# Kernel tuning notes

Hardware: AMD Instinct MI355X
Metric: run time of the kernel (lower is better)

The kernel has to match this reference:

```python
import jax, jax.numpy as jnp
import numpy as np

N_NODES = 50000
N_EDGES = 800000
F_IN = 256
HID = 64
HEADS = 4
NEG_SLOPE = 0.2


def setup_inputs() -> dict:
    key = jax.random.key(0)
    ks = jax.random.split(key, 12)
    x = jax.random.normal(ks[0], (N_NODES, F_IN), dtype=jnp.float32)
    src = jax.random.randint(ks[1], (N_EDGES,), 0, N_NODES)
    dst = jax.random.randint(ks[2], (N_EDGES,), 0, N_NODES)
    s0 = 1.0 / np.sqrt(F_IN)
    s1 = 1.0 / np.sqrt(HEADS * HID)
    W0 = jax.random.normal(ks[3], (F_IN, HEADS * HID), dtype=jnp.float32) * s0
    a_l0 = jax.random.normal(ks[4], (HEADS, HID), dtype=jnp.float32) * s1
    a_r0 = jax.random.normal(ks[5], (HEADS, HID), dtype=jnp.float32) * s1
    b0 = jnp.zeros((HEADS * HID,), dtype=jnp.float32)
    W1 = jax.random.normal(ks[6], (HEADS * HID, HEADS * HID), dtype=jnp.float32) * s1
    a_l1 = jax.random.normal(ks[7], (HEADS, HID), dtype=jnp.float32) * s1
    a_r1 = jax.random.normal(ks[8], (HEADS, HID), dtype=jnp.float32) * s1
    b1 = jnp.zeros((HEADS * HID,), dtype=jnp.float32)
    return {"x": x, "src": src, "dst": dst,
            "W0": W0, "a_l0": a_l0, "a_r0": a_r0, "b0": b0,
            "W1": W1, "a_l1": a_l1, "a_r1": a_r1, "b1": b1}


def _gat_layer(h, src, dst, W, a_l, a_r, b):
    # h: [N, F_in] -> feat: [N, H, D]
    feat = (h @ W).reshape(h.shape[0], HEADS, HID)
    el = jnp.sum(feat * a_l, axis=-1)  # [N, H]
    er = jnp.sum(feat * a_r, axis=-1)  # [N, H]
    e = jax.nn.leaky_relu(el[src] + er[dst], NEG_SLOPE)  # [E, H]
    # per-destination edge softmax (numerically stable)
    m = jax.ops.segment_max(e, dst, num_segments=N_NODES)  # [N, H]
    ex = jnp.exp(e - m[dst])
    s = jax.ops.segment_sum(ex, dst, num_segments=N_NODES)  # [N, H]
    alpha = ex / jnp.maximum(s[dst], 1e-9)  # [E, H]
    msg = feat[src] * alpha[:, :, None]  # [E, H, D]
    rst = jax.ops.segment_sum(msg, dst, num_segments=N_NODES)  # [N, H, D]
    rst = rst + b.reshape(1, HEADS, HID)
    return jax.nn.elu(rst)


def reference(x, src, dst, W0, a_l0, a_r0, b0, W1, a_l1, a_r1, b1):
    h = _gat_layer(x, src, dst, W0, a_l0, a_r0, b0)  # [N, H, D]
    h = h.reshape(N_NODES, HEADS * HID)              # flatten(1)
    h = _gat_layer(h, src, dst, W1, a_l1, a_r1, b1)  # [N, H, D]
    # list of per-head outputs h[:, i]
    return tuple(h[:, i] for i in range(HEADS))
```

## Files before the change

kernel.cpp:

```cpp
#include <hip/hip_runtime.h>
#include <math.h>

#define N_NODES 50000
#define N_EDGES 800000
#define HEADS 4
#define HID 64
#define FDIM 256
#define LDA 40
#define SCAN_CHUNK 1024
#define SCAN_NB ((N_NODES + SCAN_CHUNK - 1) / SCAN_CHUNK)

typedef __attribute__((ext_vector_type(8))) _Float16 half8;
typedef __attribute__((ext_vector_type(4))) _Float16 half4;
typedef __attribute__((ext_vector_type(4))) float f32x4;


__global__ __launch_bounds__(256) void hist_kernel(const int* __restrict__ dst,
                                                   int* __restrict__ counts, int E) {
    int i = blockIdx.x * blockDim.x + threadIdx.x;
    if (i < E) atomicAdd(&counts[dst[i]], 1);
}

__global__ __launch_bounds__(256) void scan_local(const int* __restrict__ counts,
                                                  int* __restrict__ offs,
                                                  int* __restrict__ bsum, int n) {
    __shared__ int part[256];
    const int b = blockIdx.x, t = threadIdx.x;
    const int base = b * SCAN_CHUNK + t * 4;
    int v[4];
#pragma unroll
    for (int j = 0; j < 4; j++) {
        int idx = base + j;
        v[j] = (idx < n) ? counts[idx] : 0;
    }
    int s0 = v[0], s1 = s0 + v[1], s2 = s1 + v[2], s3 = s2 + v[3];
    part[t] = s3;
    __syncthreads();
    for (int off = 1; off < 256; off <<= 1) {
        int x = (t >= off) ? part[t - off] : 0;
        __syncthreads();
        part[t] += x;
        __syncthreads();
    }
    int prefix = (t > 0) ? part[t - 1] : 0;
    int e[4] = {prefix, prefix + s0, prefix + s1, prefix + s2};
#pragma unroll
    for (int j = 0; j < 4; j++) {
        int idx = base + j;
        if (idx < n) offs[idx] = e[j];
    }
    if (t == 255) bsum[b] = part[255];
}

__global__ __launch_bounds__(64) void scan_bsum(int* __restrict__ bsum,
                                                int* __restrict__ offs, int nb, int n) {
    int lane = threadIdx.x;
    int own = (lane < nb) ? bsum[lane] : 0;
    int v = own;
    for (int off = 1; off < 64; off <<= 1) {
        int x = __shfl_up(v, off);
        if (lane >= off) v += x;
    }
    if (lane < nb) bsum[lane] = v - own;
    if (lane == nb - 1) offs[n] = v;
}

__global__ __launch_bounds__(256) void scan_add(int* __restrict__ offs,
                                                const int* __restrict__ bsum, int n) {
    const int b = blockIdx.x;
    const int p = bsum[b];
    const int base = b * SCAN_CHUNK + threadIdx.x * 4;
#pragma unroll
    for (int j = 0; j < 4; j++) {
        int idx = base + j;
        if (idx < n) offs[idx] += p;
    }
}

__global__ __launch_bounds__(256) void scatter_kernel(const int* __restrict__ src,
                                                      const int* __restrict__ dst,
                                                      const int* __restrict__ offs,
                                                      int* __restrict__ cursor,
                                                      int* __restrict__ csr_src, int E) {
    int i = blockIdx.x * blockDim.x + threadIdx.x;
    if (i < E) {
        int d = dst[i];
        int p = offs[d] + atomicAdd(&cursor[d], 1);
        csr_src[p] = src[i];
    }
}


__global__ __launch_bounds__(256) void wcast_kernel(const float* __restrict__ W0,
                                                    const float* __restrict__ W1,
                                                    _Float16* __restrict__ wt0,
                                                    _Float16* __restrict__ wt1) {
    const float* W = blockIdx.y ? W1 : W0;
    _Float16* wt = blockIdx.y ? wt1 : wt0;
    int n = blockIdx.x * 16 + (threadIdx.x >> 4);
    int k0 = (threadIdx.x & 15) * 16;
    for (int j = 0; j < 16; j++)
        wt[n * FDIM + k0 + j] = (_Float16)W[(k0 + j) * FDIM + n];
}

__global__ __launch_bounds__(256) void cast_x_kernel(const float* __restrict__ x,
                                                     _Float16* __restrict__ x16) {
    size_t i = ((size_t)blockIdx.x * 256 + threadIdx.x) * 4;
    float4 v = *(const float4*)&x[i];
    half4 h = {(_Float16)v.x, (_Float16)v.y, (_Float16)v.z, (_Float16)v.w};
    *(half4*)&x16[i] = h;
}

__global__ __launch_bounds__(256) void mfma_gemm(const _Float16* __restrict__ A16,
                                                 const _Float16* __restrict__ Bt,
                                                 const float* __restrict__ al,
                                                 const float* __restrict__ ar,
                                                 _Float16* __restrict__ feat16,
                                                 float* __restrict__ el,
                                                 float* __restrict__ er) {
    __shared__ _Float16 ash[128][LDA];
    __shared__ _Float16 bsh[128][LDA];

    const int t = threadIdx.x;
    const int m0 = blockIdx.x * 128;
    const int n0 = blockIdx.y * 128;
    const int wave = t >> 6, lane = t & 63;
    const int quad = lane >> 4, l16 = lane & 15;
    const int wr = (wave >> 1) * 64;
    const int wc = (wave & 1) * 64;

    const f32x4 zero = {0.f, 0.f, 0.f, 0.f};
    f32x4 acc[4][4];
#pragma unroll
    for (int i = 0; i < 4; i++)
#pragma unroll
        for (int j = 0; j < 4; j++) acc[i][j] = zero;

    for (int kk = 0; kk < FDIM; kk += 32) {
#pragma unroll
        for (int ii = 0; ii < 2; ii++) {
            int idx = t + ii * 256;
            int row = idx >> 2;
            int kb = (idx & 3) * 8;
            int gr = m0 + row; if (gr >= N_NODES) gr = N_NODES - 1;
            *(half8*)&ash[row][kb] = *(const half8*)&A16[(size_t)gr * FDIM + kk + kb];
            *(half8*)&bsh[row][kb] = *(const half8*)&Bt[(size_t)(n0 + row) * FDIM + kk + kb];
        }
        __syncthreads();

        half8 af[4], bf[4];
#pragma unroll
        for (int i = 0; i < 4; i++) {
            af[i] = *(half8*)&ash[wr + i * 16 + l16][quad * 8];
            bf[i] = *(half8*)&bsh[wc + i * 16 + l16][quad * 8];
        }
#pragma unroll
        for (int mt = 0; mt < 4; mt++)
#pragma unroll
            for (int nt = 0; nt < 4; nt++)
                acc[mt][nt] = __builtin_amdgcn_mfma_f32_16x16x32_f16(af[mt], bf[nt], acc[mt][nt], 0, 0, 0);
        __syncthreads();
    }

    const int h = (n0 + wc) >> 6;
    float alv[4], arv[4];
#pragma unroll
    for (int nt = 0; nt < 4; nt++) {
        alv[nt] = al[n0 + wc + nt * 16 + l16];
        arv[nt] = ar[n0 + wc + nt * 16 + l16];
    }
#pragma unroll
    for (int mt = 0; mt < 4; mt++) {
        int m = m0 + wr + mt * 16 + quad * 4;
        float pl[4] = {0.f, 0.f, 0.f, 0.f}, pr[4] = {0.f, 0.f, 0.f, 0.f};
#pragma unroll
        for (int nt = 0; nt < 4; nt++) {
            int n = n0 + wc + nt * 16 + l16;
#pragma unroll
            for (int r = 0; r < 4; r++) {
                float v = acc[mt][nt][r];
                if (m + r < N_NODES) feat16[(size_t)(m + r) * FDIM + n] = (_Float16)v;
                pl[r] += v * alv[nt];
                pr[r] += v * arv[nt];
            }
        }
#pragma unroll
        for (int r = 0; r < 4; r++) {
            float a = pl[r], b = pr[r];
            for (int off = 8; off; off >>= 1) {
                a += __shfl_down(a, off, 16);
                b += __shfl_down(b, off, 16);
            }
            if (l16 == 0 && m + r < N_NODES) {
                el[(m + r) * 4 + h] = a;
                er[(m + r) * 4 + h] = b;
            }
        }
    }
}

__global__ __launch_bounds__(256) void agg_fused(const _Float16* __restrict__ feat16,
                                                 const float* __restrict__ el,
                                                 const float* __restrict__ er,
                                                 const float* __restrict__ bias,
                                                 const int* __restrict__ offs,
                                                 const int* __restrict__ csr_src,
                                                 float* __restrict__ out,
                                                 _Float16* __restrict__ h1,
                                                 int mode) {
    const int wave = threadIdx.x >> 6;
    const int lane = threadIdx.x & 63;
    const int n = blockIdx.x * 4 + wave;
    const int head = lane >> 4;
    const int f = lane * 4;
    const int beg = offs[n];
    const int end = offs[n + 1];
    const float er_h = er[n * 4 + head];

    float4 acc0 = make_float4(0.f, 0.f, 0.f, 0.f);
    float4 acc1 = make_float4(0.f, 0.f, 0.f, 0.f);
    float ss0 = 0.f, ss1 = 0.f;

    int i = beg;
    for (; i + 3 < end; i += 4) {
        int s0 = csr_src[i], s1 = csr_src[i + 1];
        int s2 = csr_src[i + 2], s3 = csr_src[i + 3];
        float e0 = el[s0 * 4 + head] + er_h;
        float e1 = el[s1 * 4 + head] + er_h;
        float e2 = el[s2 * 4 + head] + er_h;
        float e3 = el[s3 * 4 + head] + er_h;
        half4 v0 = *(const half4*)&feat16[(size_t)s0 * FDIM + f];
        half4 v1 = *(const half4*)&feat16[(size_t)s1 * FDIM + f];
        half4 v2 = *(const half4*)&feat16[(size_t)s2 * FDIM + f];
        half4 v3 = *(const half4*)&feat16[(size_t)s3 * FDIM + f];
        e0 = (e0 > 0.f) ? e0 : 0.2f * e0;
        e1 = (e1 > 0.f) ? e1 : 0.2f * e1;
        e2 = (e2 > 0.f) ? e2 : 0.2f * e2;
        e3 = (e3 > 0.f) ? e3 : 0.2f * e3;
        float w0 = __expf(e0), w1 = __expf(e1), w2 = __expf(e2), w3 = __expf(e3);
        ss0 += w0 + w2;
        ss1 += w1 + w3;
        acc0.x += w0 * (float)v0[0] + w2 * (float)v2[0];
        acc0.y += w0 * (float)v0[1] + w2 * (float)v2[1];
        acc0.z += w0 * (float)v0[2] + w2 * (float)v2[2];
        acc0.w += w0 * (float)v0[3] + w2 * (float)v2[3];
        acc1.x += w1 * (float)v1[0] + w3 * (float)v3[0];
        acc1.y += w1 * (float)v1[1] + w3 * (float)v3[1];
        acc1.z += w1 * (float)v1[2] + w3 * (float)v3[2];
        acc1.w += w1 * (float)v1[3] + w3 * (float)v3[3];
    }
    for (; i < end; i++) {
        int s0 = csr_src[i];
        float e0 = el[s0 * 4 + head] + er_h;
        half4 v0 = *(const half4*)&feat16[(size_t)s0 * FDIM + f];
        e0 = (e0 > 0.f) ? e0 : 0.2f * e0;
        float w0 = __expf(e0);
        ss0 += w0;
        acc0.x += w0 * (float)v0[0];
        acc0.y += w0 * (float)v0[1];
        acc0.z += w0 * (float)v0[2];
        acc0.w += w0 * (float)v0[3];
    }

    float S = fmaxf(ss0 + ss1, 1e-9f);
    float inv = 1.f / S;
    float4 bv = *(const float4*)&bias[f];
    float r0 = (acc0.x + acc1.x) * inv + bv.x;
    float r1 = (acc0.y + acc1.y) * inv + bv.y;
    float r2 = (acc0.z + acc1.z) * inv + bv.z;
    float r3 = (acc0.w + acc1.w) * inv + bv.w;
    r0 = (r0 > 0.f) ? r0 : expm1f(r0);
    r1 = (r1 > 0.f) ? r1 : expm1f(r1);
    r2 = (r2 > 0.f) ? r2 : expm1f(r2);
    r3 = (r3 > 0.f) ? r3 : expm1f(r3);

    if (mode) {
        const int d = (lane & 15) * 4;
        float4 rv = make_float4(r0, r1, r2, r3);
        *(float4*)&out[(size_t)head * N_NODES * HID + (size_t)n * HID + d] = rv;
    } else {
        half4 hv = {(_Float16)r0, (_Float16)r1, (_Float16)r2, (_Float16)r3};
        *(half4*)&h1[(size_t)n * FDIM + f] = hv;
    }
}


extern "C" void kernel_launch(void* const* d_in, const int* in_sizes, int n_in,
                              void* d_out, int out_size, void* d_ws, size_t ws_size,
                              hipStream_t stream) {
    const float* x   = (const float*)d_in[0];
    const int*   src = (const int*)d_in[1];
    const int*   dst = (const int*)d_in[2];
    const float* W0  = (const float*)d_in[3];
    const float* al0 = (const float*)d_in[4];
    const float* ar0 = (const float*)d_in[5];
    const float* b0  = (const float*)d_in[6];
    const float* W1  = (const float*)d_in[7];
    const float* al1 = (const float*)d_in[8];
    const float* ar1 = (const float*)d_in[9];
    const float* b1  = (const float*)d_in[10];
    float* out = (float*)d_out;

    _Float16* x16h1 = (_Float16*)d_out;

    _Float16* feat16 = (_Float16*)d_ws;
    _Float16* wt0 = feat16 + (size_t)N_NODES * FDIM;
    _Float16* wt1 = wt0 + FDIM * FDIM;
    float* el    = (float*)(wt1 + FDIM * FDIM);
    float* er    = el + N_NODES * HEADS;
    int* counts  = (int*)(er + N_NODES * HEADS);
    int* cursor  = counts + N_NODES;
    int* offs    = cursor + N_NODES;
    int* bsum    = offs + 50016;
    int* csr_src = bsum + 64;

    hipMemsetAsync(counts, 0, 2 * N_NODES * sizeof(int), stream);
    wcast_kernel<<<dim3(16, 2), 256, 0, stream>>>(W0, W1, wt0, wt1);
    cast_x_kernel<<<N_NODES * FDIM / 1024, 256, 0, stream>>>(x, x16h1);
    hist_kernel<<<(N_EDGES + 255) / 256, 256, 0, stream>>>(dst, counts, N_EDGES);
    scan_local<<<SCAN_NB, 256, 0, stream>>>(counts, offs, bsum, N_NODES);
    scan_bsum<<<1, 64, 0, stream>>>(bsum, offs, SCAN_NB, N_NODES);
    scan_add<<<SCAN_NB, 256, 0, stream>>>(offs, bsum, N_NODES);
    scatter_kernel<<<(N_EDGES + 255) / 256, 256, 0, stream>>>(src, dst, offs, cursor, csr_src, N_EDGES);

    dim3 ggrid((N_NODES + 127) / 128, FDIM / 128);

    mfma_gemm<<<ggrid, 256, 0, stream>>>(x16h1, wt0, al0, ar0, feat16, el, er);
    agg_fused<<<N_NODES / 4, 256, 0, stream>>>(feat16, el, er, b0, offs, csr_src,
                                               out, x16h1, 0);

    mfma_gemm<<<ggrid, 256, 0, stream>>>(x16h1, wt1, al1, ar1, feat16, el, er);
    agg_fused<<<N_NODES / 4, 256, 0, stream>>>(feat16, el, er, b1, offs, csr_src,
                                               out, x16h1, 1);
}
```

Baseline: 385.9 us.

## Slab feature layout, fuse x cast into GEMM, split aggregation per slab

```diff
diff --git a/kernel.cpp b/kernel.cpp
--- a/kernel.cpp
+++ b/kernel.cpp
@@ -9,6 +9,7 @@
 #define LDA 40
 #define SCAN_CHUNK 1024
 #define SCAN_NB ((N_NODES + SCAN_CHUNK - 1) / SCAN_CHUNK)
+#define SLAB ((size_t)N_NODES * 32)
 
 typedef __attribute__((ext_vector_type(8))) _Float16 half8;
 typedef __attribute__((ext_vector_type(4))) _Float16 half4;
@@ -103,15 +104,9 @@
         wt[n * FDIM + k0 + j] = (_Float16)W[(k0 + j) * FDIM + n];
 }
 
-__global__ __launch_bounds__(256) void cast_x_kernel(const float* __restrict__ x,
-                                                     _Float16* __restrict__ x16) {
-    size_t i = ((size_t)blockIdx.x * 256 + threadIdx.x) * 4;
-    float4 v = *(const float4*)&x[i];
-    half4 h = {(_Float16)v.x, (_Float16)v.y, (_Float16)v.z, (_Float16)v.w};
-    *(half4*)&x16[i] = h;
-}
-
-__global__ __launch_bounds__(256) void mfma_gemm(const _Float16* __restrict__ A16,
+template <int AMODE>
+__global__ __launch_bounds__(256) void mfma_gemm(const float* __restrict__ A32,
+                                                 const _Float16* __restrict__ A16,
                                                  const _Float16* __restrict__ Bt,
                                                  const float* __restrict__ al,
                                                  const float* __restrict__ ar,
@@ -137,13 +132,32 @@
         for (int j = 0; j < 4; j++) acc[i][j] = zero;
 
     for (int kk = 0; kk < FDIM; kk += 32) {
+        if constexpr (AMODE == 0) {
+            const int ar_ = t >> 3, ac = (t & 7) * 4;
+#pragma unroll
+            for (int rr = 0; rr < 4; rr++) {
+                int row = ar_ + rr * 32;
+                int gr = m0 + row; if (gr >= N_NODES) gr = N_NODES - 1;
+                float4 v = *(const float4*)&A32[(size_t)gr * FDIM + kk + ac];
+                half4 h = {(_Float16)v.x, (_Float16)v.y, (_Float16)v.z, (_Float16)v.w};
+                *(half4*)&ash[row][ac] = h;
+            }
+        } else {
+            const int s0 = kk >> 5;
+#pragma unroll
+            for (int ii = 0; ii < 2; ii++) {
+                int idx = t + ii * 256;
+                int row = idx >> 2;
+                int kb = (idx & 3) * 8;
+                int gr = m0 + row; if (gr >= N_NODES) gr = N_NODES - 1;
+                *(half8*)&ash[row][kb] = *(const half8*)&A16[(size_t)s0 * SLAB + (size_t)gr * 32 + kb];
+            }
+        }
 #pragma unroll
         for (int ii = 0; ii < 2; ii++) {
             int idx = t + ii * 256;
             int row = idx >> 2;
             int kb = (idx & 3) * 8;
-            int gr = m0 + row; if (gr >= N_NODES) gr = N_NODES - 1;
-            *(half8*)&ash[row][kb] = *(const half8*)&A16[(size_t)gr * FDIM + kk + kb];
             *(half8*)&bsh[row][kb] = *(const half8*)&Bt[(size_t)(n0 + row) * FDIM + kk + kb];
         }
         __syncthreads();
@@ -176,10 +190,12 @@
 #pragma unroll
         for (int nt = 0; nt < 4; nt++) {
             int n = n0 + wc + nt * 16 + l16;
+            int sl = n >> 5, within = n & 31;
 #pragma unroll
             for (int r = 0; r < 4; r++) {
                 float v = acc[mt][nt][r];
-                if (m + r < N_NODES) feat16[(size_t)(m + r) * FDIM + n] = (_Float16)v;
+                if (m + r < N_NODES)
+                    feat16[(size_t)sl * SLAB + (size_t)(m + r) * 32 + within] = (_Float16)v;
                 pl[r] += v * alv[nt];
                 pr[r] += v * arv[nt];
             }
@@ -199,7 +215,7 @@
     }
 }
 
-__global__ __launch_bounds__(256) void agg_fused(const _Float16* __restrict__ feat16,
+__global__ __launch_bounds__(512) void agg_fused(const _Float16* __restrict__ feat16,
                                                  const float* __restrict__ el,
                                                  const float* __restrict__ er,
                                                  const float* __restrict__ bias,
@@ -210,77 +226,58 @@
                                                  int mode) {
     const int wave = threadIdx.x >> 6;
     const int lane = threadIdx.x & 63;
-    const int n = blockIdx.x * 4 + wave;
-    const int head = lane >> 4;
-    const int f = lane * 4;
+    const int sl = blockIdx.x & 7;
+    const int n = (blockIdx.x >> 3) * 8 + wave;
+    const int head = sl >> 1;
+    const int half32 = (sl & 1) * 32;
+    const int slot = lane >> 3;
+    const int fl = (lane & 7) * 4;
     const int beg = offs[n];
     const int end = offs[n + 1];
     const float er_h = er[n * 4 + head];
-
-    float4 acc0 = make_float4(0.f, 0.f, 0.f, 0.f);
-    float4 acc1 = make_float4(0.f, 0.f, 0.f, 0.f);
-    float ss0 = 0.f, ss1 = 0.f;
-
-    int i = beg;
-    for (; i + 3 < end; i += 4) {
-        int s0 = csr_src[i], s1 = csr_src[i + 1];
-        int s2 = csr_src[i + 2], s3 = csr_src[i + 3];
-        float e0 = el[s0 * 4 + head] + er_h;
-        float e1 = el[s1 * 4 + head] + er_h;
-        float e2 = el[s2 * 4 + head] + er_h;
-        float e3 = el[s3 * 4 + head] + er_h;
-        half4 v0 = *(const half4*)&feat16[(size_t)s0 * FDIM + f];
-        half4 v1 = *(const half4*)&feat16[(size_t)s1 * FDIM + f];
-        half4 v2 = *(const half4*)&feat16[(size_t)s2 * FDIM + f];
-        half4 v3 = *(const half4*)&feat16[(size_t)s3 * FDIM + f];
-        e0 = (e0 > 0.f) ? e0 : 0.2f * e0;
-        e1 = (e1 > 0.f) ? e1 : 0.2f * e1;
-        e2 = (e2 > 0.f) ? e2 : 0.2f * e2;
-        e3 = (e3 > 0.f) ? e3 : 0.2f * e3;
-        float w0 = __expf(e0), w1 = __expf(e1), w2 = __expf(e2), w3 = __expf(e3);
-        ss0 += w0 + w2;
-        ss1 += w1 + w3;
-        acc0.x += w0 * (float)v0[0] + w2 * (float)v2[0];
-        acc0.y += w0 * (float)v0[1] + w2 * (float)v2[1];
-        acc0.z += w0 * (float)v0[2] + w2 * (float)v2[2];
-        acc0.w += w0 * (float)v0[3] + w2 * (float)v2[3];
-        acc1.x += w1 * (float)v1[0] + w3 * (float)v3[0];
-        acc1.y += w1 * (float)v1[1] + w3 * (float)v3[1];
-        acc1.z += w1 * (float)v1[2] + w3 * (float)v3[2];
-        acc1.w += w1 * (float)v1[3] + w3 * (float)v3[3];
-    }
-    for (; i < end; i++) {
-        int s0 = csr_src[i];
-        float e0 = el[s0 * 4 + head] + er_h;
-        half4 v0 = *(const half4*)&feat16[(size_t)s0 * FDIM + f];
-        e0 = (e0 > 0.f) ? e0 : 0.2f * e0;
-        float w0 = __expf(e0);
-        ss0 += w0;
-        acc0.x += w0 * (float)v0[0];
-        acc0.y += w0 * (float)v0[1];
-        acc0.z += w0 * (float)v0[2];
-        acc0.w += w0 * (float)v0[3];
-    }
-
-    float S = fmaxf(ss0 + ss1, 1e-9f);
-    float inv = 1.f / S;
-    float4 bv = *(const float4*)&bias[f];
-    float r0 = (acc0.x + acc1.x) * inv + bv.x;
-    float r1 = (acc0.y + acc1.y) * inv + bv.y;
-    float r2 = (acc0.z + acc1.z) * inv + bv.z;
-    float r3 = (acc0.w + acc1.w) * inv + bv.w;
-    r0 = (r0 > 0.f) ? r0 : expm1f(r0);
-    r1 = (r1 > 0.f) ? r1 : expm1f(r1);
-    r2 = (r2 > 0.f) ? r2 : expm1f(r2);
-    r3 = (r3 > 0.f) ? r3 : expm1f(r3);
-
-    if (mode) {
-        const int d = (lane & 15) * 4;
-        float4 rv = make_float4(r0, r1, r2, r3);
-        *(float4*)&out[(size_t)head * N_NODES * HID + (size_t)n * HID + d] = rv;
-    } else {
-        half4 hv = {(_Float16)r0, (_Float16)r1, (_Float16)r2, (_Float16)r3};
-        *(half4*)&h1[(size_t)n * FDIM + f] = hv;
+    const _Float16* slab = feat16 + (size_t)sl * SLAB;
+
+    float4 acc = make_float4(0.f, 0.f, 0.f, 0.f);
+    float ssum = 0.f;
+    for (int i = beg + slot; i < end; i += 8) {
+        int s = csr_src[i];
+        float e = el[s * 4 + head] + er_h;
+        half4 v = *(const half4*)&slab[(size_t)s * 32 + fl];
+        e = (e > 0.f) ? e : 0.2f * e;
+        float w = __expf(e);
+        ssum += w;
+        acc.x += w * (float)v[0];
+        acc.y += w * (float)v[1];
+        acc.z += w * (float)v[2];
+        acc.w += w * (float)v[3];
+    }
+#pragma unroll
+    for (int m = 8; m <= 32; m <<= 1) {
+        acc.x += __shfl_xor(acc.x, m);
+        acc.y += __shfl_xor(acc.y, m);
+        acc.z += __shfl_xor(acc.z, m);
+        acc.w += __shfl_xor(acc.w, m);
+        ssum += __shfl_xor(ssum, m);
+    }
+
+    if (slot == 0) {
+        float inv = 1.f / fmaxf(ssum, 1e-9f);
+        float4 bv = *(const float4*)&bias[head * HID + half32 + fl];
+        float r0 = acc.x * inv + bv.x;
+        float r1 = acc.y * inv + bv.y;
+        float r2 = acc.z * inv + bv.z;
+        float r3 = acc.w * inv + bv.w;
+        r0 = (r0 > 0.f) ? r0 : expm1f(r0);
+        r1 = (r1 > 0.f) ? r1 : expm1f(r1);
+        r2 = (r2 > 0.f) ? r2 : expm1f(r2);
+        r3 = (r3 > 0.f) ? r3 : expm1f(r3);
+        if (mode) {
+            float4 rv = make_float4(r0, r1, r2, r3);
+            *(float4*)&out[(size_t)head * N_NODES * HID + (size_t)n * HID + half32 + fl] = rv;
+        } else {
+            half4 hv = {(_Float16)r0, (_Float16)r1, (_Float16)r2, (_Float16)r3};
+            *(half4*)&h1[(size_t)sl * SLAB + (size_t)n * 32 + fl] = hv;
+        }
     }
 }
 
@@ -301,7 +298,7 @@
     const float* b1  = (const float*)d_in[10];
     float* out = (float*)d_out;
 
-    _Float16* x16h1 = (_Float16*)d_out;
+    _Float16* h1 = (_Float16*)d_out;
 
     _Float16* feat16 = (_Float16*)d_ws;
     _Float16* wt0 = feat16 + (size_t)N_NODES * FDIM;
@@ -316,7 +313,6 @@
 
     hipMemsetAsync(counts, 0, 2 * N_NODES * sizeof(int), stream);
     wcast_kernel<<<dim3(16, 2), 256, 0, stream>>>(W0, W1, wt0, wt1);
-    cast_x_kernel<<<N_NODES * FDIM / 1024, 256, 0, stream>>>(x, x16h1);
     hist_kernel<<<(N_EDGES + 255) / 256, 256, 0, stream>>>(dst, counts, N_EDGES);
     scan_local<<<SCAN_NB, 256, 0, stream>>>(counts, offs, bsum, N_NODES);
     scan_bsum<<<1, 64, 0, stream>>>(bsum, offs, SCAN_NB, N_NODES);
@@ -324,12 +320,13 @@
     scatter_kernel<<<(N_EDGES + 255) / 256, 256, 0, stream>>>(src, dst, offs, cursor, csr_src, N_EDGES);
 
     dim3 ggrid((N_NODES + 127) / 128, FDIM / 128);
-
-    mfma_gemm<<<ggrid, 256, 0, stream>>>(x16h1, wt0, al0, ar0, feat16, el, er);
-    agg_fused<<<N_NODES / 4, 256, 0, stream>>>(feat16, el, er, b0, offs, csr_src,
-                                               out, x16h1, 0);
-
-    mfma_gemm<<<ggrid, 256, 0, stream>>>(x16h1, wt1, al1, ar1, feat16, el, er);
-    agg_fused<<<N_NODES / 4, 256, 0, stream>>>(feat16, el, er, b1, offs, csr_src,
-                                               out, x16h1, 1);
-}
+    const int agg_grid = (N_NODES / 8) * 8;
+
+    mfma_gemm<0><<<ggrid, 256, 0, stream>>>(x, nullptr, wt0, al0, ar0, feat16, el, er);
+    agg_fused<<<agg_grid, 512, 0, stream>>>(feat16, el, er, b0, offs, csr_src,
+                                            out, h1, 0);
+
+    mfma_gemm<1><<<ggrid, 256, 0, stream>>>(nullptr, h1, wt1, al1, ar1, feat16, el, er);
+    agg_fused<<<agg_grid, 512, 0, stream>>>(feat16, el, er, b1, offs, csr_src,
+                                            out, h1, 1);
+}
```

Measured after the change: 598.2 us. 55.0% more time.
